# Optimization experiments

Hardware: AMD Instinct MI355X
Metric: run time of the kernel (lower is better)

Reference implementation:

```python
import jax, jax.numpy as jnp
import numpy as np

N_BINS = 256
HOP = 80


def _gru(xs, Wih, Whh, bih, bhh, reverse=False):
    """Single-layer unidirectional GRU, PyTorch gate layout (r, z, n).
    xs: (T, B, I); Wih: (3H, I); Whh: (3H, H). Returns (T, B, H)."""
    H = Whh.shape[1]
    gi = jnp.einsum('tbi,gi->tbg', xs, Wih) + bih  # precompute input projections

    def step(h, gi_t):
        gh = h @ Whh.T + bhh
        ir, iz, inn = jnp.split(gi_t, 3, axis=-1)
        hr, hz, hn = jnp.split(gh, 3, axis=-1)
        r = jax.nn.sigmoid(ir + hr)
        z = jax.nn.sigmoid(iz + hz)
        n = jnp.tanh(inn + r * hn)
        h_new = (1.0 - z) * n + z * h
        return h_new, h_new

    h0 = jnp.zeros((xs.shape[1], H), xs.dtype)
    _, ys = jax.lax.scan(step, h0, gi, reverse=reverse)
    return ys


def _quantize(w):
    # continuous [-1, 1] -> bin index in [0, N_BINS-1]
    return jnp.clip(jnp.floor((w + 1.0) * (N_BINS / 2)), 0, N_BINS - 1).astype(jnp.int32)


def _forward(x, y, p):
    # --- encode: 2-layer bidirectional GRU over mel frames ---
    c = x
    for l in ('m0', 'm1'):
        f = _gru(c, p[l + 'f_Wih'], p[l + 'f_Whh'], p[l + 'f_bih'], p[l + 'f_bhh'])
        bwd = _gru(c, p[l + 'b_Wih'], p[l + 'b_Whh'], p[l + 'b_bih'], p[l + 'b_bhh'], reverse=True)
        c = jnp.concatenate([f, bwd], axis=-1)  # (t_m, b, 2*dim_enc)
    # nearest-neighbor upsample in time (matches F.interpolate default 'nearest')
    c = jnp.repeat(c, HOP, axis=0)  # (t_w, b, 2*dim_enc)

    # --- teacher forcing: shift waveform right, vectorize via embedding ---
    b = x.shape[1]
    w = jnp.concatenate([jnp.zeros((1, b), y.dtype), y[:-1]], axis=0)
    e = p['E'][_quantize(w)]  # (t_w, b, dim_vec)

    # --- wav GRU + projection + GELU ---
    o = _gru(jnp.concatenate([e, c], axis=-1), p['w_Wih'], p['w_Whh'], p['w_bih'], p['w_bhh'])
    o = jax.nn.gelu(o @ p['Wp'].T + p['bp'], approximate=False)  # (t_w, b, dim_proj)

    # --- categorical neg log prob over quantized targets ---
    logits = o @ p['Wd'].T + p['bd']  # (t_w, b, N_BINS)
    logp = jax.nn.log_softmax(logits, axis=-1)
    tgt = _quantize(y)
    nll = -jnp.mean(jnp.take_along_axis(logp, tgt[..., None], axis=-1))
    return nll


def setup_inputs() -> dict:
    key = jax.random.key(0)
    ks = iter(jax.random.split(key, 64))

    def rn(shape, s=0.08):
        return jax.random.normal(next(ks), shape, jnp.float32) * s

    t_m, b, dm = 32, 4, 80
    de, dv, dd, dp = 128, 256, 896, 512
    d = {}
    d['x'] = jax.random.normal(next(ks), (t_m, b, dm), jnp.float32)
    d['y'] = jax.random.uniform(next(ks), (t_m * HOP, b), jnp.float32, minval=-1.0, maxval=1.0)
    for name, i in [('m0f', dm), ('m0b', dm), ('m1f', 2 * de), ('m1b', 2 * de)]:
        d[name + '_Wih'] = rn((3 * de, i))
        d[name + '_Whh'] = rn((3 * de, de))
        d[name + '_bih'] = rn((3 * de,))
        d[name + '_bhh'] = rn((3 * de,))
    d['w_Wih'] = rn((3 * dd, 2 * de + dv))
    d['w_Whh'] = rn((3 * dd, dd))
    d['w_bih'] = rn((3 * dd,))
    d['w_bhh'] = rn((3 * dd,))
    d['Wp'] = rn((dp, dd))
    d['bp'] = rn((dp,))
    d['E'] = rn((N_BINS, dv))
    d['Wd'] = rn((N_BINS, dp))
    d['bd'] = rn((N_BINS,))
    return d


def reference(x, y, m0f_Wih, m0f_Whh, m0f_bih, m0f_bhh, m0b_Wih, m0b_Whh, m0b_bih, m0b_bhh,
              m1f_Wih, m1f_Whh, m1f_bih, m1f_bhh, m1b_Wih, m1b_Whh, m1b_bih, m1b_bhh,
              w_Wih, w_Whh, w_bih, w_bhh, Wp, bp, E, Wd, bd):
    p = dict(m0f_Wih=m0f_Wih, m0f_Whh=m0f_Whh, m0f_bih=m0f_bih, m0f_bhh=m0f_bhh,
             m0b_Wih=m0b_Wih, m0b_Whh=m0b_Whh, m0b_bih=m0b_bih, m0b_bhh=m0b_bhh,
             m1f_Wih=m1f_Wih, m1f_Whh=m1f_Whh, m1f_bih=m1f_bih, m1f_bhh=m1f_bhh,
             m1b_Wih=m1b_Wih, m1b_Whh=m1b_Whh, m1b_bih=m1b_bih, m1b_bhh=m1b_bhh,
             w_Wih=w_Wih, w_Whh=w_Whh, w_bih=w_bih, w_bhh=w_bhh,
             Wp=Wp, bp=bp, E=E, Wd=Wd, bd=bd)
    return _forward(x, y, p)
```

## Files before the change

kernel.cpp:

```cpp
#include <hip/hip_runtime.h>
#include <stdint.h>
#include <math.h>

typedef __attribute__((ext_vector_type(8))) short bf16x8;
typedef __attribute__((ext_vector_type(4))) float f32x4;
typedef __attribute__((ext_vector_type(4))) unsigned int u32x4;

#define BATCH 4
#define T_M 32
#define DE 128
#define T_W 2560
#define NWG 28

__device__ __forceinline__ float b2f(unsigned short h) {
  return __uint_as_float(((unsigned int)h) << 16);
}
__device__ __forceinline__ unsigned short f2b(float f) {
  unsigned int u = __float_as_uint(f);
  u = u + 0x7fffu + ((u >> 16) & 1u);
  return (unsigned short)(u >> 16);
}
__device__ __forceinline__ float blo(unsigned int u){ return __uint_as_float(u << 16); }
__device__ __forceinline__ float bhi(unsigned int u){ return __uint_as_float(u & 0xffff0000u); }
__device__ __forceinline__ float sigm(float x){ return 1.f / (1.f + __expf(-x)); }
__device__ __forceinline__ float gelu_exact(float x){ return 0.5f * x * (1.f + erff(x * 0.70710678118654752f)); }

__global__ __launch_bounds__(256) void k_cast(const float* __restrict__ src,
                                              unsigned short* __restrict__ dst, int n)
{
  int i = blockIdx.x * 256 + threadIdx.x;
  if (i < n) dst[i] = f2b(src[i]);
}

__global__ __launch_bounds__(256) void k_prep_whh(const float* __restrict__ whh,
                                                  unsigned short* __restrict__ out)
{
  int idx = blockIdx.x * 256 + threadIdx.x;
  if (idx >= 224 * 28 * 512) return;
  int j    = idx & 7;
  int r16  = (idx >> 3) & 15;
  int quad = (idx >> 7) & 3;
  int kc   = (idx >> 9) % 28;
  int G    = (idx >> 9) / 28;
  unsigned short val = 0;
  if (r16 < 12) {
    int row = (r16 >> 2) * 896 + G * 4 + (r16 & 3);
    int col = kc * 32 + quad * 8 + j;
    val = f2b(whh[(size_t)row * 896 + col]);
  }
  out[idx] = val;
}

__global__ __launch_bounds__(384) void k_gi_enc(
    const float* __restrict__ in, const float* __restrict__ Wih,
    const float* __restrict__ bih, float* __restrict__ out, int K)
{
  __shared__ float in_s[256];
  int tb = blockIdx.x;
  for (int i = threadIdx.x; i < K; i += 384) in_s[i] = in[tb * K + i];
  __syncthreads();
  int row = threadIdx.x;
  float acc = bih[row];
  const float* wr = Wih + row * K;
  for (int k = 0; k < K; ++k) acc += in_s[k] * wr[k];
  out[tb * 384 + row] = acc;
}

__global__ __launch_bounds__(512) void k_scan_enc(
    const float* __restrict__ gi_f, const float* __restrict__ gi_b,
    const float* __restrict__ whh_f, const float* __restrict__ bhh_f,
    const float* __restrict__ whh_b, const float* __restrict__ bhh_b,
    float* __restrict__ c_out)
{
  const int dir = blockIdx.x, tid = threadIdx.x;
  const float* gi  = dir ? gi_b  : gi_f;
  const float* whh = dir ? whh_b : whh_f;
  const float* bhh = dir ? bhh_b : bhh_f;
  __shared__ unsigned short h_s[BATCH][DE + 8];
  __shared__ float gh_s[384][4];
  __shared__ float bhh_s[384];
  for (int i = tid; i < 384; i += 512) bhh_s[i] = bhh[i];
  for (int i = tid; i < BATCH * (DE + 8); i += 512) ((unsigned short*)h_s)[i] = 0;
  __syncthreads();
  for (int s = 0; s < T_M; ++s) {
    int t = dir ? (T_M - 1 - s) : s;
    #pragma unroll
    for (int k3 = 0; k3 < 3; ++k3) {
      int d = tid + 512 * k3;
      int row = d >> 2, b = d & 3;
      const float* wr = whh + row * DE;
      float acc = 0.f;
      for (int j = 0; j < DE; j += 8) {
        float4 w0 = *(const float4*)(wr + j);
        float4 w1 = *(const float4*)(wr + j + 4);
        uint4  hv = *(const uint4*)&h_s[b][j];
        acc += w0.x * blo(hv.x) + w0.y * bhi(hv.x) + w0.z * blo(hv.y) + w0.w * bhi(hv.y);
        acc += w1.x * blo(hv.z) + w1.y * bhi(hv.z) + w1.z * blo(hv.w) + w1.w * bhi(hv.w);
      }
      gh_s[row][b] = acc + bhh_s[row];
    }
    __syncthreads();
    {
      int u = tid >> 2, b = tid & 3;
      const float* git = gi + (t * BATCH + b) * 384;
      float r = sigm(git[u] + gh_s[u][b]);
      float z = sigm(git[DE + u] + gh_s[DE + u][b]);
      float n = tanhf(git[2 * DE + u] + r * gh_s[2 * DE + u][b]);
      float hold = b2f(h_s[b][u]);
      float hnew = (1.f - z) * n + z * hold;
      c_out[(t * BATCH + b) * 256 + dir * DE + u] = hnew;
      h_s[b][u] = f2b(hnew);
    }
    __syncthreads();
  }
}

__global__ __launch_bounds__(256) void k_build_X(
    const float* __restrict__ y, const float* __restrict__ E,
    const float* __restrict__ c1, unsigned short* __restrict__ X)
{
  int t = blockIdx.x, c = threadIdx.x;
  int tm = t / 80;
  #pragma unroll
  for (int b = 0; b < BATCH; ++b) {
    float w = (t == 0) ? 0.f : y[(t - 1) * BATCH + b];
    int q = (int)floorf((w + 1.f) * 128.f);
    q = q < 0 ? 0 : (q > 255 ? 255 : q);
    unsigned short* xb = X + (size_t)(t * BATCH + b) * 512;
    xb[c]       = f2b(E[q * 256 + c]);
    xb[256 + c] = f2b(c1[(tm * BATCH + b) * 256 + c]);
  }
}

__global__ __launch_bounds__(256) void k_mgemm(
    const unsigned short* __restrict__ A, const unsigned short* __restrict__ B,
    const float* __restrict__ bias, void* __restrict__ C,
    int M, int N, int K, int act, int c_bf16)
{
  __shared__ unsigned short As[128][40];
  __shared__ unsigned short Bs[128][40];
  const int tid = threadIdx.x;
  const int m0 = blockIdx.x * 128, n0 = blockIdx.y * 128;
  const int lane = tid & 63, wave = tid >> 6;
  const int wy = wave >> 1, wx = wave & 1;
  const int row16 = lane & 15, quad = lane >> 4;
  const int sr = tid >> 1, sc = (tid & 1) * 16;
  f32x4 acc[4][4] = {};
  for (int kt = 0; kt < K; kt += 32) {
    uint4 av  = *(const uint4*)(A + (size_t)(m0 + sr) * K + kt + sc);
    uint4 av2 = *(const uint4*)(A + (size_t)(m0 + sr) * K + kt + sc + 8);
    uint4 bv  = *(const uint4*)(B + (size_t)(n0 + sr) * K + kt + sc);
    uint4 bv2 = *(const uint4*)(B + (size_t)(n0 + sr) * K + kt + sc + 8);
    __syncthreads();
    *(uint4*)&As[sr][sc] = av; *(uint4*)&As[sr][sc + 8] = av2;
    *(uint4*)&Bs[sr][sc] = bv; *(uint4*)&Bs[sr][sc + 8] = bv2;
    __syncthreads();
    bf16x8 af[4], bf[4];
    #pragma unroll
    for (int i = 0; i < 4; ++i) af[i] = *(const bf16x8*)&As[wy * 64 + i * 16 + row16][quad * 8];
    #pragma unroll
    for (int j = 0; j < 4; ++j) bf[j] = *(const bf16x8*)&Bs[wx * 64 + j * 16 + row16][quad * 8];
    #pragma unroll
    for (int i = 0; i < 4; ++i)
      #pragma unroll
      for (int j = 0; j < 4; ++j)
        acc[i][j] = __builtin_amdgcn_mfma_f32_16x16x32_bf16(af[i], bf[j], acc[i][j], 0, 0, 0);
  }
  #pragma unroll
  for (int i = 0; i < 4; ++i) {
    #pragma unroll
    for (int j = 0; j < 4; ++j) {
      int col = n0 + wx * 64 + j * 16 + row16;
      float bs = bias[col];
      #pragma unroll
      for (int r = 0; r < 4; ++r) {
        int row = m0 + wy * 64 + i * 16 + quad * 4 + r;
        float v = acc[i][j][r] + bs;
        if (act) v = gelu_exact(v);
        if (c_bf16) ((unsigned short*)C)[(size_t)row * N + col] = f2b(v);
        else        ((float*)C)[(size_t)row * N + col] = v;
      }
    }
  }
}

__global__ __launch_bounds__(512, 1) void k_wav_rnn(
    const unsigned short* __restrict__ whh_p,
    const float* __restrict__ bhh,
    const unsigned short* __restrict__ gi,
    unsigned int* __restrict__ hslots,
    unsigned int* __restrict__ O32)
{
  const int wg = blockIdx.x, tid = threadIdx.x;
  const int lane = tid & 63, wave = tid >> 6;
  const int G = wg * 8 + wave;

  __shared__ unsigned short h_lds[4][912];
  __shared__ float phh[8][3][4][4];

  const int r16 = lane & 15, quad = lane >> 4, bb = lane & 3;
  const int fu = (lane >> 2) & 3, fb = lane & 3;

  bf16x8 wf[28];
  {
    const bf16x8* W8 = (const bf16x8*)whh_p + (size_t)G * 28 * 64;
    #pragma unroll
    for (int kc = 0; kc < 28; ++kc)
      wf[kc] = W8[(kc * 4 + quad) * 16 + r16];
  }

  const float br_ = bhh[G * 4 + fu];
  const float bz_ = bhh[896 + G * 4 + fu];
  const float bn_ = bhh[1792 + G * 4 + fu];
  float hprev = 0.f;
  const unsigned short* gbase = gi + G * 4 + fu;
  unsigned short cr = gbase[(size_t)fb * 2688];
  unsigned short cz = gbase[(size_t)fb * 2688 + 896];
  unsigned short cn = gbase[(size_t)fb * 2688 + 1792];

  const int l56 = (lane < 56) ? lane : (lane - 56);
  const int p0 = wave * 112 + l56;
  const int p1 = p0 + 56;
  const int pb0 = p0 / 224, pG0 = p0 - pb0 * 224;
  const int pb1 = p1 / 224, pG1 = p1 - pb1 * 224;

  const unsigned long long base0 = (unsigned long long)hslots;
  const unsigned long long base1 = base0 + 14336ull;

  for (int t = 0; t < T_W; ++t) {
    const unsigned long long hb = (t & 1) ? base1 : base0;
    unsigned long long a0 = hb + ((unsigned long long)p0 << 4);
    unsigned long long a1 = hb + ((unsigned long long)p1 << 4);
    u32x4 s0, s1;
    const unsigned int tg = (unsigned int)t;
    unsigned int bad;
    do {
      asm volatile(
        "global_load_dwordx4 %0, %2, off sc0 sc1\n"
        "global_load_dwordx4 %1, %3, off sc0 sc1\n"
        "s_waitcnt vmcnt(0)"
        : "=&v"(s0), "=&v"(s1)
        : "v"(a0), "v"(a1)
        : "memory");
      bad = (s0.z ^ tg) | (s1.z ^ tg);
    } while (__any(bad != 0));

    if (lane < 56) {
      *(uint2*)&h_lds[pb0][pG0 * 4] = make_uint2(s0.x, s0.y);
      *(uint2*)&h_lds[pb1][pG1 * 4] = make_uint2(s1.x, s1.y);
    }
    __syncthreads();

    int tn = (t + 1 < T_W) ? (t + 1) : t;
    const unsigned short* gp = gbase + (size_t)(tn * 4 + fb) * 2688;
    unsigned short nr_ = gp[0], nz_ = gp[896], nn_ = gp[1792];

    f32x4 ac0 = {}, ac1 = {}, ac2 = {}, ac3 = {};
    #pragma unroll
    for (int kc = 0; kc < 28; kc += 4) {
      bf16x8 h0 = *(const bf16x8*)&h_lds[bb][(kc + 0) * 32 + quad * 8];
      bf16x8 h1 = *(const bf16x8*)&h_lds[bb][(kc + 1) * 32 + quad * 8];
      bf16x8 h2 = *(const bf16x8*)&h_lds[bb][(kc + 2) * 32 + quad * 8];
      bf16x8 h3 = *(const bf16x8*)&h_lds[bb][(kc + 3) * 32 + quad * 8];
      ac0 = __builtin_amdgcn_mfma_f32_16x16x32_bf16(wf[kc + 0], h0, ac0, 0, 0, 0);
      ac1 = __builtin_amdgcn_mfma_f32_16x16x32_bf16(wf[kc + 1], h1, ac1, 0, 0, 0);
      ac2 = __builtin_amdgcn_mfma_f32_16x16x32_bf16(wf[kc + 2], h2, ac2, 0, 0, 0);
      ac3 = __builtin_amdgcn_mfma_f32_16x16x32_bf16(wf[kc + 3], h3, ac3, 0, 0, 0);
    }
    f32x4 ac;
    ac[0] = ac0[0] + ac1[0] + ac2[0] + ac3[0];
    ac[1] = ac0[1] + ac1[1] + ac2[1] + ac3[1];
    ac[2] = ac0[2] + ac1[2] + ac2[2] + ac3[2];
    ac[3] = ac0[3] + ac1[3] + ac2[3] + ac3[3];

    if (r16 < 4 && quad < 3)
      *(f32x4*)&phh[wave][quad][r16][0] = ac;
    asm volatile("s_waitcnt lgkmcnt(0)" ::: "memory");

    float pr = phh[wave][0][fb][fu];
    float pz = phh[wave][1][fb][fu];
    float pn = phh[wave][2][fb][fu];
    float r = sigm(b2f(cr) + br_ + pr);
    float z = sigm(b2f(cz) + bz_ + pz);
    float n = tanhf(b2f(cn) + bn_ + r * pn);
    float h = (1.f - z) * n + z * hprev;
    hprev = h;
    unsigned int hu = f2b(h);
    cr = nr_; cz = nz_; cn = nn_;

    int b = lane & 3;
    unsigned int u0v = (unsigned int)__shfl((int)hu, 0 + b);
    unsigned int u1v = (unsigned int)__shfl((int)hu, 4 + b);
    unsigned int u2v = (unsigned int)__shfl((int)hu, 8 + b);
    unsigned int u3v = (unsigned int)__shfl((int)hu, 12 + b);
    if (lane < 4) {
      u32x4 pkt;
      pkt.x = (u0v & 0xffffu) | (u1v << 16);
      pkt.y = (u2v & 0xffffu) | (u3v << 16);
      pkt.z = (unsigned int)(t + 1);
      pkt.w = 0u;
      *(uint2*)(O32 + (size_t)(t * 4 + b) * 448 + G * 2) = make_uint2(pkt.x, pkt.y);
      unsigned long long sa = (((t + 1) & 1) ? base1 : base0)
                            + (unsigned long long)((b * 224 + G) << 4);
      asm volatile("global_store_dwordx4 %0, %1, off sc0 sc1"
                   :: "v"(sa), "v"(pkt) : "memory");
    }
    __syncthreads();
  }
}

__global__ __launch_bounds__(256) void k_nll(
    const float* __restrict__ logits, const float* __restrict__ y,
    float* __restrict__ acc)
{
  int wid = threadIdx.x >> 6, lane = threadIdx.x & 63;
  int row = blockIdx.x * 4 + wid;
  const float* lr = logits + (size_t)row * 256;
  float v0 = lr[lane], v1 = lr[lane + 64], v2 = lr[lane + 128], v3 = lr[lane + 192];
  float mx = fmaxf(fmaxf(v0, v1), fmaxf(v2, v3));
  for (int off = 32; off > 0; off >>= 1) mx = fmaxf(mx, __shfl_xor(mx, off));
  float se = __expf(v0 - mx) + __expf(v1 - mx) + __expf(v2 - mx) + __expf(v3 - mx);
  for (int off = 32; off > 0; off >>= 1) se += __shfl_xor(se, off);
  if (lane == 0) {
    float w = y[row];
    int q = (int)floorf((w + 1.f) * 128.f);
    q = q < 0 ? 0 : (q > 255 ? 255 : q);
    float contrib = (logf(se) + mx) - lr[q];
    atomicAdd(acc, contrib);
  }
}

__global__ void k_final(const float* __restrict__ acc, float* __restrict__ out) {
  out[0] = acc[0] * (1.f / 10240.f);
}

extern "C" void kernel_launch(void* const* d_in, const int* in_sizes, int n_in,
                              void* d_out, int out_size, void* d_ws, size_t ws_size,
                              hipStream_t stream)
{
  const float* x       = (const float*)d_in[0];
  const float* y       = (const float*)d_in[1];
  const float* m0f_Wih = (const float*)d_in[2];
  const float* m0f_Whh = (const float*)d_in[3];
  const float* m0f_bih = (const float*)d_in[4];
  const float* m0f_bhh = (const float*)d_in[5];
  const float* m0b_Wih = (const float*)d_in[6];
  const float* m0b_Whh = (const float*)d_in[7];
  const float* m0b_bih = (const float*)d_in[8];
  const float* m0b_bhh = (const float*)d_in[9];
  const float* m1f_Wih = (const float*)d_in[10];
  const float* m1f_Whh = (const float*)d_in[11];
  const float* m1f_bih = (const float*)d_in[12];
  const float* m1f_bhh = (const float*)d_in[13];
  const float* m1b_Wih = (const float*)d_in[14];
  const float* m1b_Whh = (const float*)d_in[15];
  const float* m1b_bih = (const float*)d_in[16];
  const float* m1b_bhh = (const float*)d_in[17];
  const float* w_Wih   = (const float*)d_in[18];
  const float* w_Whh   = (const float*)d_in[19];
  const float* w_bih   = (const float*)d_in[20];
  const float* w_bhh   = (const float*)d_in[21];
  const float* Wp      = (const float*)d_in[22];
  const float* bp      = (const float*)d_in[23];
  const float* E       = (const float*)d_in[24];
  const float* Wd      = (const float*)d_in[25];
  const float* bd      = (const float*)d_in[26];

  char* ws = (char*)d_ws;
  size_t off = 0;
  auto alloc = [&](size_t bytes) -> void* {
    void* p = ws + off;
    off += (bytes + 255) & ~(size_t)255;
    return p;
  };
  float*        nacc   = (float*)alloc(64);
  unsigned int* hslots = (unsigned int*)alloc(2 * 896 * 16);
  size_t misc_bytes = off;

  float* c0   = (float*)alloc((size_t)32 * 4 * 256 * 4);
  float* c1   = (float*)alloc((size_t)32 * 4 * 256 * 4);
  float* gi0f = (float*)alloc((size_t)32 * 4 * 384 * 4);
  float* gi0b = (float*)alloc((size_t)32 * 4 * 384 * 4);
  float* gi1f = (float*)alloc((size_t)32 * 4 * 384 * 4);
  float* gi1b = (float*)alloc((size_t)32 * 4 * 384 * 4);
  unsigned short* X     = (unsigned short*)alloc((size_t)10240 * 512 * 2);
  unsigned short* gi_w  = (unsigned short*)alloc((size_t)10240 * 2688 * 2);
  unsigned int*   O32   = (unsigned int*)alloc((size_t)10240 * 448 * 4);
  unsigned short* O2    = (unsigned short*)alloc((size_t)10240 * 512 * 2);
  float*          LG    = (float*)alloc((size_t)10240 * 256 * 4);
  unsigned short* Wih_b = (unsigned short*)alloc((size_t)2688 * 512 * 2);
  unsigned short* Whh_p = (unsigned short*)alloc((size_t)224 * 28 * 512 * 2);
  unsigned short* Wp_b  = (unsigned short*)alloc((size_t)512 * 896 * 2);
  unsigned short* Wd_b  = (unsigned short*)alloc((size_t)256 * 512 * 2);

  hipMemsetAsync(d_ws, 0, misc_bytes, stream);

  k_cast<<<(2688 * 512 + 255) / 256, 256, 0, stream>>>(w_Wih, Wih_b, 2688 * 512);
  k_cast<<<(512 * 896 + 255) / 256, 256, 0, stream>>>(Wp, Wp_b, 512 * 896);
  k_cast<<<(256 * 512 + 255) / 256, 256, 0, stream>>>(Wd, Wd_b, 256 * 512);
  k_prep_whh<<<(224 * 28 * 512 + 255) / 256, 256, 0, stream>>>(w_Whh, Whh_p);

  k_gi_enc<<<128, 384, 0, stream>>>(x, m0f_Wih, m0f_bih, gi0f, 80);
  k_gi_enc<<<128, 384, 0, stream>>>(x, m0b_Wih, m0b_bih, gi0b, 80);
  k_scan_enc<<<2, 512, 0, stream>>>(gi0f, gi0b, m0f_Whh, m0f_bhh, m0b_Whh, m0b_bhh, c0);
  k_gi_enc<<<128, 384, 0, stream>>>(c0, m1f_Wih, m1f_bih, gi1f, 256);
  k_gi_enc<<<128, 384, 0, stream>>>(c0, m1b_Wih, m1b_bih, gi1b, 256);
  k_scan_enc<<<2, 512, 0, stream>>>(gi1f, gi1b, m1f_Whh, m1f_bhh, m1b_Whh, m1b_bhh, c1);

  k_build_X<<<2560, 256, 0, stream>>>(y, E, c1, X);
  k_mgemm<<<dim3(80, 21), 256, 0, stream>>>(X, Wih_b, w_bih, (void*)gi_w,
                                            10240, 2688, 512, 0, 1);

  k_wav_rnn<<<NWG, 512, 0, stream>>>(Whh_p, w_bhh, gi_w, hslots, O32);

  k_mgemm<<<dim3(80, 4), 256, 0, stream>>>((const unsigned short*)O32, Wp_b, bp,
                                           (void*)O2, 10240, 512, 896, 1, 1);
  k_mgemm<<<dim3(80, 2), 256, 0, stream>>>(O2, Wd_b, bd, (void*)LG,
                                           10240, 256, 512, 0, 0);
  k_nll<<<2560, 256, 0, stream>>>(LG, y, nacc);
  k_final<<<1, 1, 0, stream>>>(nacc, (float*)d_out);
}
```

Before: 6.151 ms.

## Pack gate inputs per group, double-buffer h in LDS, drop trailing barrier

The input-projection GEMM now writes its output in a per-timestep, per-group packed layout so each recurrent wave reads its r/z/n gate inputs from one contiguous 96-byte chunk. The prefetch of the next step's inputs is issued before the LDS barrier. The h staging buffer in LDS is double-buffered by step parity, which removes the second __syncthreads per timestep. Sigmoid and tanh now use hardware reciprocal and exp approximations; the tanh is clamped to stay in range but is less accurate, and dropping the barrier relies on parity buffering plus the global flag handshake for correctness.

```diff
diff --git a/kernel.cpp b/kernel.cpp
--- a/kernel.cpp
+++ b/kernel.cpp
@@ -22,7 +22,13 @@
 }
 __device__ __forceinline__ float blo(unsigned int u){ return __uint_as_float(u << 16); }
 __device__ __forceinline__ float bhi(unsigned int u){ return __uint_as_float(u & 0xffff0000u); }
-__device__ __forceinline__ float sigm(float x){ return 1.f / (1.f + __expf(-x)); }
+__device__ __forceinline__ float sigm(float x){
+  return __builtin_amdgcn_rcpf(1.f + __expf(-x));
+}
+__device__ __forceinline__ float tanh_fast(float x){
+  float x2 = fminf(fmaxf(x + x, -30.f), 30.f);
+  return 1.f - 2.f * __builtin_amdgcn_rcpf(__expf(x2) + 1.f);
+}
 __device__ __forceinline__ float gelu_exact(float x){ return 0.5f * x * (1.f + erff(x * 0.70710678118654752f)); }
 
 __global__ __launch_bounds__(256) void k_cast(const float* __restrict__ src,
@@ -105,7 +111,7 @@
       const float* git = gi + (t * BATCH + b) * 384;
       float r = sigm(git[u] + gh_s[u][b]);
       float z = sigm(git[DE + u] + gh_s[DE + u][b]);
-      float n = tanhf(git[2 * DE + u] + r * gh_s[2 * DE + u][b]);
+      float n = tanh_fast(git[2 * DE + u] + r * gh_s[2 * DE + u][b]);
       float hold = b2f(h_s[b][u]);
       float hnew = (1.f - z) * n + z * hold;
       c_out[(t * BATCH + b) * 256 + dir * DE + u] = hnew;
@@ -135,7 +141,7 @@
 __global__ __launch_bounds__(256) void k_mgemm(
     const unsigned short* __restrict__ A, const unsigned short* __restrict__ B,
     const float* __restrict__ bias, void* __restrict__ C,
-    int M, int N, int K, int act, int c_bf16)
+    int M, int N, int K, int act, int c_bf16, int swz)
 {
   __shared__ unsigned short As[128][40];
   __shared__ unsigned short Bs[128][40];
@@ -177,8 +183,16 @@
         int row = m0 + wy * 64 + i * 16 + quad * 4 + r;
         float v = acc[i][j][r] + bs;
         if (act) v = gelu_exact(v);
-        if (c_bf16) ((unsigned short*)C)[(size_t)row * N + col] = f2b(v);
-        else        ((float*)C)[(size_t)row * N + col] = v;
+        if (swz) {
+          int t = row >> 2, b = row & 3;
+          int g = col / 896, rem = col - g * 896;
+          int G = rem >> 2, u = rem & 3;
+          ((unsigned short*)C)[(size_t)(t * 224 + G) * 48 + g * 16 + b * 4 + u] = f2b(v);
+        } else if (c_bf16) {
+          ((unsigned short*)C)[(size_t)row * N + col] = f2b(v);
+        } else {
+          ((float*)C)[(size_t)row * N + col] = v;
+        }
       }
     }
   }
@@ -187,7 +201,7 @@
 __global__ __launch_bounds__(512, 1) void k_wav_rnn(
     const unsigned short* __restrict__ whh_p,
     const float* __restrict__ bhh,
-    const unsigned short* __restrict__ gi,
+    const unsigned short* __restrict__ gp_,
     unsigned int* __restrict__ hslots,
     unsigned int* __restrict__ O32)
 {
@@ -195,7 +209,7 @@
   const int lane = tid & 63, wave = tid >> 6;
   const int G = wg * 8 + wave;
 
-  __shared__ unsigned short h_lds[4][912];
+  __shared__ unsigned short h_lds[2][4][912];
   __shared__ float phh[8][3][4][4];
 
   const int r16 = lane & 15, quad = lane >> 4, bb = lane & 3;
@@ -213,10 +227,8 @@
   const float bz_ = bhh[896 + G * 4 + fu];
   const float bn_ = bhh[1792 + G * 4 + fu];
   float hprev = 0.f;
-  const unsigned short* gbase = gi + G * 4 + fu;
-  unsigned short cr = gbase[(size_t)fb * 2688];
-  unsigned short cz = gbase[(size_t)fb * 2688 + 896];
-  unsigned short cn = gbase[(size_t)fb * 2688 + 1792];
+  const unsigned short* gl0 = gp_ + (size_t)G * 48 + fb * 4 + fu;
+  unsigned short cr = gl0[0], cz = gl0[16], cn = gl0[32];
 
   const int l56 = (lane < 56) ? lane : (lane - 56);
   const int p0 = wave * 112 + l56;
@@ -245,23 +257,23 @@
       bad = (s0.z ^ tg) | (s1.z ^ tg);
     } while (__any(bad != 0));
 
+    int tn = (t + 1 < T_W) ? (t + 1) : t;
+    const unsigned short* gp = gp_ + (size_t)tn * 10752 + G * 48 + fb * 4 + fu;
+    unsigned short nr_ = gp[0], nz_ = gp[16], nn_ = gp[32];
+
     if (lane < 56) {
-      *(uint2*)&h_lds[pb0][pG0 * 4] = make_uint2(s0.x, s0.y);
-      *(uint2*)&h_lds[pb1][pG1 * 4] = make_uint2(s1.x, s1.y);
+      *(uint2*)&h_lds[t & 1][pb0][pG0 * 4] = make_uint2(s0.x, s0.y);
+      *(uint2*)&h_lds[t & 1][pb1][pG1 * 4] = make_uint2(s1.x, s1.y);
     }
     __syncthreads();
 
-    int tn = (t + 1 < T_W) ? (t + 1) : t;
-    const unsigned short* gp = gbase + (size_t)(tn * 4 + fb) * 2688;
-    unsigned short nr_ = gp[0], nz_ = gp[896], nn_ = gp[1792];
-
     f32x4 ac0 = {}, ac1 = {}, ac2 = {}, ac3 = {};
     #pragma unroll
     for (int kc = 0; kc < 28; kc += 4) {
-      bf16x8 h0 = *(const bf16x8*)&h_lds[bb][(kc + 0) * 32 + quad * 8];
-      bf16x8 h1 = *(const bf16x8*)&h_lds[bb][(kc + 1) * 32 + quad * 8];
-      bf16x8 h2 = *(const bf16x8*)&h_lds[bb][(kc + 2) * 32 + quad * 8];
-      bf16x8 h3 = *(const bf16x8*)&h_lds[bb][(kc + 3) * 32 + quad * 8];
+      bf16x8 h0 = *(const bf16x8*)&h_lds[t & 1][bb][(kc + 0) * 32 + quad * 8];
+      bf16x8 h1 = *(const bf16x8*)&h_lds[t & 1][bb][(kc + 1) * 32 + quad * 8];
+      bf16x8 h2 = *(const bf16x8*)&h_lds[t & 1][bb][(kc + 2) * 32 + quad * 8];
+      bf16x8 h3 = *(const bf16x8*)&h_lds[t & 1][bb][(kc + 3) * 32 + quad * 8];
       ac0 = __builtin_amdgcn_mfma_f32_16x16x32_bf16(wf[kc + 0], h0, ac0, 0, 0, 0);
       ac1 = __builtin_amdgcn_mfma_f32_16x16x32_bf16(wf[kc + 1], h1, ac1, 0, 0, 0);
       ac2 = __builtin_amdgcn_mfma_f32_16x16x32_bf16(wf[kc + 2], h2, ac2, 0, 0, 0);
@@ -282,7 +294,7 @@
     float pn = phh[wave][2][fb][fu];
     float r = sigm(b2f(cr) + br_ + pr);
     float z = sigm(b2f(cz) + bz_ + pz);
-    float n = tanhf(b2f(cn) + bn_ + r * pn);
+    float n = tanh_fast(b2f(cn) + bn_ + r * pn);
     float h = (1.f - z) * n + z * hprev;
     hprev = h;
     unsigned int hu = f2b(h);
@@ -299,13 +311,12 @@
       pkt.y = (u2v & 0xffffu) | (u3v << 16);
       pkt.z = (unsigned int)(t + 1);
       pkt.w = 0u;
-      *(uint2*)(O32 + (size_t)(t * 4 + b) * 448 + G * 2) = make_uint2(pkt.x, pkt.y);
       unsigned long long sa = (((t + 1) & 1) ? base1 : base0)
                             + (unsigned long long)((b * 224 + G) << 4);
       asm volatile("global_store_dwordx4 %0, %1, off sc0 sc1"
                    :: "v"(sa), "v"(pkt) : "memory");
-    }
-    __syncthreads();
+      *(uint2*)(O32 + (size_t)(t * 4 + b) * 448 + G * 2) = make_uint2(pkt.x, pkt.y);
+    }
   }
 }
 
@@ -384,7 +395,7 @@
   float* gi1f = (float*)alloc((size_t)32 * 4 * 384 * 4);
   float* gi1b = (float*)alloc((size_t)32 * 4 * 384 * 4);
   unsigned short* X     = (unsigned short*)alloc((size_t)10240 * 512 * 2);
-  unsigned short* gi_w  = (unsigned short*)alloc((size_t)10240 * 2688 * 2);
+  unsigned short* gpack = (unsigned short*)alloc((size_t)2560 * 224 * 48 * 2);
   unsigned int*   O32   = (unsigned int*)alloc((size_t)10240 * 448 * 4);
   unsigned short* O2    = (unsigned short*)alloc((size_t)10240 * 512 * 2);
   float*          LG    = (float*)alloc((size_t)10240 * 256 * 4);
@@ -408,15 +419,15 @@
   k_scan_enc<<<2, 512, 0, stream>>>(gi1f, gi1b, m1f_Whh, m1f_bhh, m1b_Whh, m1b_bhh, c1);
 
   k_build_X<<<2560, 256, 0, stream>>>(y, E, c1, X);
-  k_mgemm<<<dim3(80, 21), 256, 0, stream>>>(X, Wih_b, w_bih, (void*)gi_w,
-                                            10240, 2688, 512, 0, 1);
-
-  k_wav_rnn<<<NWG, 512, 0, stream>>>(Whh_p, w_bhh, gi_w, hslots, O32);
+  k_mgemm<<<dim3(80, 21), 256, 0, stream>>>(X, Wih_b, w_bih, (void*)gpack,
+                                            10240, 2688, 512, 0, 1, 1);
+
+  k_wav_rnn<<<NWG, 512, 0, stream>>>(Whh_p, w_bhh, gpack, hslots, O32);
 
   k_mgemm<<<dim3(80, 4), 256, 0, stream>>>((const unsigned short*)O32, Wp_b, bp,
-                                           (void*)O2, 10240, 512, 896, 1, 1);
+                                           (void*)O2, 10240, 512, 896, 1, 1, 0);
   k_mgemm<<<dim3(80, 2), 256, 0, stream>>>(O2, Wd_b, bd, (void*)LG,
-                                           10240, 256, 512, 0, 0);
+                                           10240, 256, 512, 0, 0, 0);
   k_nll<<<2560, 256, 0, stream>>>(LG, y, nacc);
   k_final<<<1, 1, 0, stream>>>(nacc, (float*)d_out);
 }
```

Result: faster. 5.992 ms (-2.6%).
